# Kernel optimization log

Measured on AMD Instinct MI355X. Metric: run time of the kernel, lower is better.

The kernel has to match this reference:

```python
import jax, jax.numpy as jnp
import numpy as np

N = 50000
E = 600000
D = 128
BN_EPS = 1e-5
GIN_EPS = 0.0  # init_eps=0, not learned


def setup_inputs() -> dict:
    key = jax.random.key(0)
    ks = jax.random.split(key, 8)
    x = jax.random.normal(ks[0], (N, D), dtype=jnp.float32)
    edge_index = jax.random.randint(ks[1], (2, E), 0, N, dtype=jnp.int64)
    s = 1.0 / np.sqrt(D)
    w1 = jax.random.uniform(ks[2], (D, D), jnp.float32, -s, s)
    b1 = jax.random.uniform(ks[3], (D,), jnp.float32, -s, s)
    w2 = jax.random.uniform(ks[4], (D, D), jnp.float32, -s, s)
    b2 = jax.random.uniform(ks[5], (D,), jnp.float32, -s, s)
    gamma = jnp.ones((D,), jnp.float32)
    beta = jnp.zeros((D,), jnp.float32)
    return {"x": x, "edge_index": edge_index, "w1": w1, "b1": b1,
            "w2": w2, "b2": b2, "gamma": gamma, "beta": beta}


def reference(x, edge_index, w1, b1, w2, b2, gamma, beta):
    src, dst = edge_index[0], edge_index[1]
    # GINConv sum aggregation: out[i] = sum_{(j,i) in E} x[j]
    agg = jax.ops.segment_sum(x[src], dst, num_segments=N)  # [N, D]
    h = (1.0 + GIN_EPS) * x + agg
    # 2-layer MLP (Linear-ReLU-Linear)
    h = jax.nn.relu(h @ w1 + b1)
    h = h @ w2 + b2
    # training-mode BatchNorm over nodes (biased variance)
    mean = jnp.mean(h, axis=0)
    var = jnp.var(h, axis=0)
    h = (h - mean) * jax.lax.rsqrt(var + BN_EPS) * gamma + beta
    h = jax.nn.relu(h)
    # residual (in_dim == out_dim); dropout p=0.0 -> identity
    return x + h
```

## Files before the change

### kernel.cpp

```cpp
#include <hip/hip_runtime.h>

#define NN 50000
#define EE 600000
#define DD 128
#define MTILE 64
#define LDSTR 136
#define MAXDEG 64
#define NSLICE 32

typedef __attribute__((ext_vector_type(8))) short short8;
typedef __attribute__((ext_vector_type(4))) float f32x4;

static __device__ __forceinline__ unsigned short f2bf(float f) {
    unsigned int u = __float_as_uint(f);
    u += 0x7FFF + ((u >> 16) & 1);
    return (unsigned short)(u >> 16);
}
static __device__ __forceinline__ float bflo(unsigned int u) {
    return __uint_as_float(u << 16);
}
static __device__ __forceinline__ float bfhi(unsigned int u) {
    return __uint_as_float(u & 0xFFFF0000u);
}


__global__ __launch_bounds__(256) void k_prep(const float* __restrict__ w1,
                                              const float* __restrict__ w2,
                                              const float* __restrict__ x,
                                              unsigned short* __restrict__ wt,
                                              unsigned int* __restrict__ xb) {
    int tid = blockIdx.x * 256 + threadIdx.x;
    if (tid < 32768) {
        int w = tid >> 14, idx = tid & 16383;
        int k = idx >> 7, n = idx & 127;
        const float* src = w ? w2 : w1;
        wt[w * 16384 + n * 128 + k] = f2bf(src[k * 128 + n]);
    }
    int xi = tid - 32768;
    if (xi >= 0 && xi < NN * DD / 2) {
        float2 v = ((const float2*)x)[xi];
        xb[xi] = (unsigned int)f2bf(v.x) | ((unsigned int)f2bf(v.y) << 16);
    }
}


__global__ void k_scatter(const int* __restrict__ ei, int* __restrict__ cursor,
                          int* __restrict__ srcPad) {
    int e = blockIdx.x * blockDim.x + threadIdx.x;
    if (e < EE) {
        int s = ei[e];
        int d = ei[EE + e];
        int pos = atomicAdd(&cursor[d], 1);
        if (pos < MAXDEG) srcPad[(d << 6) + pos] = s;
    }
}


__global__ __launch_bounds__(256) void k_agg(const unsigned int* __restrict__ xb,
                                             const int* __restrict__ cursor,
                                             const int* srcPad,
                                             unsigned int* h0) {
    int wave = (blockIdx.x * blockDim.x + threadIdx.x) >> 6;
    int lane = threadIdx.x & 63;
    if (wave >= NN) return;
    int cnt = cursor[wave];
    if (cnt > MAXDEG) cnt = MAXDEG;
    int sv = srcPad[(wave << 6) + lane];
    unsigned int self = xb[(wave << 6) + lane];
    float ax = bflo(self), ay = bfhi(self);
    int j = 0;
    for (; j + 4 <= cnt; j += 4) {
        int a0 = __shfl(sv, j, 64);
        int a1 = __shfl(sv, j + 1, 64);
        int a2 = __shfl(sv, j + 2, 64);
        int a3 = __shfl(sv, j + 3, 64);
        unsigned int u0 = xb[(a0 << 6) + lane];
        unsigned int u1 = xb[(a1 << 6) + lane];
        unsigned int u2 = xb[(a2 << 6) + lane];
        unsigned int u3 = xb[(a3 << 6) + lane];
        ax += bflo(u0) + bflo(u1) + bflo(u2) + bflo(u3);
        ay += bfhi(u0) + bfhi(u1) + bfhi(u2) + bfhi(u3);
    }
    for (; j < cnt; ++j) {
        int s = __shfl(sv, j, 64);
        unsigned int u = xb[(s << 6) + lane];
        ax += bflo(u);
        ay += bfhi(u);
    }
    h0[(wave << 6) + lane] = (unsigned int)f2bf(ax) | ((unsigned int)f2bf(ay) << 16);
}


__global__ __launch_bounds__(256) void k_gemm(const unsigned short* __restrict__ A,
                                              const unsigned short* __restrict__ W,
                                              const float* __restrict__ bias,
                                              unsigned short* __restrict__ Cb,
                                              float* __restrict__ Cf,
                                              float* __restrict__ priv,
                                              int relu_bf16) {
    __shared__ __align__(16) unsigned short As[MTILE * LDSTR];
    __shared__ __align__(16) unsigned short Ws[128 * LDSTR];
    int t = threadIdx.x;
    int row0 = blockIdx.x * MTILE;

    #pragma unroll
    for (int i = 0; i < 8; ++i) {
        int idx = i * 256 + t;
        int r = idx >> 4, c = idx & 15;
        *(short8*)&Ws[r * LDSTR + c * 8] = *(const short8*)&W[r * 128 + c * 8];
    }
    #pragma unroll
    for (int i = 0; i < 4; ++i) {
        int idx = i * 256 + t;
        int r = idx >> 4, c = idx & 15;
        int gr = row0 + r;
        short8 v = (short8)0;
        if (gr < NN) v = *(const short8*)&A[gr * 128 + c * 8];
        *(short8*)&As[r * LDSTR + c * 8] = v;
    }
    __syncthreads();

    int lane = t & 63, wid = t >> 6;
    int m = lane & 15, quad = lane >> 4;
    f32x4 acc[8];
    #pragma unroll
    for (int i = 0; i < 8; ++i) acc[i] = (f32x4)0.f;

    #pragma unroll
    for (int kc = 0; kc < 4; ++kc) {
        int ko = kc * 32 + quad * 8;
        short8 af = *(const short8*)&As[(wid * 16 + m) * LDSTR + ko];
        #pragma unroll
        for (int nt = 0; nt < 8; ++nt) {
            short8 bfr = *(const short8*)&Ws[(nt * 16 + m) * LDSTR + ko];
            acc[nt] = __builtin_amdgcn_mfma_f32_16x16x32_bf16(af, bfr, acc[nt], 0, 0, 0);
        }
    }

    if (relu_bf16) {
        #pragma unroll
        for (int nt = 0; nt < 8; ++nt) {
            int col = nt * 16 + m;
            float bv = bias[col];
            #pragma unroll
            for (int r = 0; r < 4; ++r) {
                int gr = row0 + wid * 16 + quad * 4 + r;
                if (gr < NN) Cb[gr * 128 + col] = f2bf(fmaxf(acc[nt][r] + bv, 0.f));
            }
        }
    } else {
        float* myslice = priv + ((blockIdx.x * 4 + wid) & (NSLICE - 1)) * 2 * DD;
        #pragma unroll
        for (int nt = 0; nt < 8; ++nt) {
            int col = nt * 16 + m;
            float bv = bias[col];
            float s = 0.f, sq = 0.f;
            #pragma unroll
            for (int r = 0; r < 4; ++r) {
                int gr = row0 + wid * 16 + quad * 4 + r;
                if (gr < NN) {
                    float v = acc[nt][r] + bv;
                    Cf[gr * 128 + col] = v;
                    s += v;
                    sq += v * v;
                }
            }
            s  += __shfl_down(s, 32, 64);  sq += __shfl_down(sq, 32, 64);
            s  += __shfl_down(s, 16, 64);  sq += __shfl_down(sq, 16, 64);
            if (quad == 0) {
                atomicAdd(&myslice[col], s);
                atomicAdd(&myslice[DD + col], sq);
            }
        }
    }
}


__global__ __launch_bounds__(256) void k_bnred(const float* __restrict__ priv,
                                               float* __restrict__ stats) {
    int t = threadIdx.x;
    float acc = 0.f;
    #pragma unroll
    for (int s = 0; s < NSLICE; ++s) acc += priv[s * 2 * DD + t];
    stats[t] = acc;
}


__global__ __launch_bounds__(256) void k_final(const float* __restrict__ x,
                                               float* __restrict__ h,
                                               const float* __restrict__ stats,
                                               const float* __restrict__ gamma,
                                               const float* __restrict__ beta) {
    __shared__ float ssc[DD], ssh[DD];
    int t = threadIdx.x;
    if (t < DD) {
        float mean = stats[t] * (1.0f / NN);
        float var = fmaxf(stats[DD + t] * (1.0f / NN) - mean * mean, 0.f);
        float sc = gamma[t] * rsqrtf(var + 1e-5f);
        ssc[t] = sc;
        ssh[t] = beta[t] - mean * sc;
    }
    __syncthreads();
    int idx = blockIdx.x * 256 + t;
    if (idx >= NN * DD / 4) return;
    int c0 = (idx & 31) * 4;
    float4 hv = ((const float4*)h)[idx];
    float4 xv = ((const float4*)x)[idx];
    float4 o;
    o.x = xv.x + fmaxf(fmaf(hv.x, ssc[c0 + 0], ssh[c0 + 0]), 0.f);
    o.y = xv.y + fmaxf(fmaf(hv.y, ssc[c0 + 1], ssh[c0 + 1]), 0.f);
    o.z = xv.z + fmaxf(fmaf(hv.z, ssc[c0 + 2], ssh[c0 + 2]), 0.f);
    o.w = xv.w + fmaxf(fmaf(hv.w, ssc[c0 + 3], ssh[c0 + 3]), 0.f);
    ((float4*)h)[idx] = o;
}

extern "C" void kernel_launch(void* const* d_in, const int* in_sizes, int n_in,
                              void* d_out, int out_size, void* d_ws, size_t ws_size,
                              hipStream_t stream) {
    (void)in_sizes; (void)n_in; (void)out_size; (void)ws_size;
    const float* x     = (const float*)d_in[0];
    const int*   ei    = (const int*)d_in[1];
    const float* w1    = (const float*)d_in[2];
    const float* b1    = (const float*)d_in[3];
    const float* w2    = (const float*)d_in[4];
    const float* b2    = (const float*)d_in[5];
    const float* gamma = (const float*)d_in[6];
    const float* beta  = (const float*)d_in[7];
    float* out = (float*)d_out;

    char* wsb = (char*)d_ws;
    int*   cursor  = (int*)(wsb);
    int*   srcPad  = (int*)(wsb + 0x40000);
    unsigned int*   h0w = (unsigned int*)srcPad;
    unsigned short* h0b = (unsigned short*)srcPad;
    unsigned int*   xb  = (unsigned int*)(wsb + 0xD00000);
    unsigned short* h1b = (unsigned short*)xb;
    unsigned short* wt  = (unsigned short*)(wsb + 0x1940000);
    float* stats   = (float*)(wsb + 0x1960000);
    float* priv    = (float*)(wsb + 0x1961000);

    (void)hipMemsetAsync(cursor, 0, NN * sizeof(int), stream);
    (void)hipMemsetAsync(priv, 0, NSLICE * 2 * DD * sizeof(float), stream);

    k_prep<<<(32768 + NN * DD / 2 + 255) / 256, 256, 0, stream>>>(w1, w2, x, wt, xb);
    k_scatter<<<(EE + 255) / 256, 256, 0, stream>>>(ei, cursor, srcPad);
    k_agg<<<(NN * 64 + 255) / 256, 256, 0, stream>>>(xb, cursor, srcPad, h0w);
    k_gemm<<<(NN + MTILE - 1) / MTILE, 256, 0, stream>>>(h0b, wt, b1, h1b, nullptr, nullptr, 1);
    k_gemm<<<(NN + MTILE - 1) / MTILE, 256, 0, stream>>>(h1b, wt + 16384, b2, nullptr, out, priv, 0);
    k_bnred<<<1, 256, 0, stream>>>(priv, stats);
    k_final<<<(NN * DD / 4 + 255) / 256, 256, 0, stream>>>(x, out, stats, gamma, beta);
}
```

Before: 211.9 us.

## Fuse scatter into prep, enlarge GEMM tile, store bf16 pre-BN, fold BN reduce

Merges the edge-scatter kernel into the prep kernel and folds the BN slice reduction into the final kernel, removing two launches. The GEMM tile grows to 128 rows so each wave computes two 16-row MFMA tiles that share the same weight fragments. The second GEMM now writes its pre-BN output as bf16 to workspace instead of fp32 to the output buffer, which cuts intermediate traffic at some precision cost. The aggregation loop is unrolled by 8 for more loads in flight, and the final kernel processes four float4 elements per thread.

```diff
diff --git a/kernel.cpp b/kernel.cpp
--- a/kernel.cpp
+++ b/kernel.cpp
@@ -3,7 +3,7 @@
 #define NN 50000
 #define EE 600000
 #define DD 128
-#define MTILE 64
+#define MTILE 128
 #define LDSTR 136
 #define MAXDEG 64
 #define NSLICE 32
@@ -27,9 +27,18 @@
 __global__ __launch_bounds__(256) void k_prep(const float* __restrict__ w1,
                                               const float* __restrict__ w2,
                                               const float* __restrict__ x,
+                                              const int* __restrict__ ei,
+                                              int* __restrict__ cursor,
+                                              int* __restrict__ srcPad,
                                               unsigned short* __restrict__ wt,
                                               unsigned int* __restrict__ xb) {
     int tid = blockIdx.x * 256 + threadIdx.x;
+    if (tid < EE) {
+        int s = ei[tid];
+        int d = ei[EE + tid];
+        int pos = atomicAdd(&cursor[d], 1);
+        if (pos < MAXDEG) srcPad[(d << 6) + pos] = s;
+    }
     if (tid < 32768) {
         int w = tid >> 14, idx = tid & 16383;
         int k = idx >> 7, n = idx & 127;
@@ -40,18 +49,6 @@
     if (xi >= 0 && xi < NN * DD / 2) {
         float2 v = ((const float2*)x)[xi];
         xb[xi] = (unsigned int)f2bf(v.x) | ((unsigned int)f2bf(v.y) << 16);
-    }
-}
-
-
-__global__ void k_scatter(const int* __restrict__ ei, int* __restrict__ cursor,
-                          int* __restrict__ srcPad) {
-    int e = blockIdx.x * blockDim.x + threadIdx.x;
-    if (e < EE) {
-        int s = ei[e];
-        int d = ei[EE + e];
-        int pos = atomicAdd(&cursor[d], 1);
-        if (pos < MAXDEG) srcPad[(d << 6) + pos] = s;
     }
 }
 
@@ -69,15 +66,25 @@
     unsigned int self = xb[(wave << 6) + lane];
     float ax = bflo(self), ay = bfhi(self);
     int j = 0;
+    for (; j + 8 <= cnt; j += 8) {
+        int a0 = __shfl(sv, j, 64),     a1 = __shfl(sv, j + 1, 64);
+        int a2 = __shfl(sv, j + 2, 64), a3 = __shfl(sv, j + 3, 64);
+        int a4 = __shfl(sv, j + 4, 64), a5 = __shfl(sv, j + 5, 64);
+        int a6 = __shfl(sv, j + 6, 64), a7 = __shfl(sv, j + 7, 64);
+        unsigned int u0 = xb[(a0 << 6) + lane], u1 = xb[(a1 << 6) + lane];
+        unsigned int u2 = xb[(a2 << 6) + lane], u3 = xb[(a3 << 6) + lane];
+        unsigned int u4 = xb[(a4 << 6) + lane], u5 = xb[(a5 << 6) + lane];
+        unsigned int u6 = xb[(a6 << 6) + lane], u7 = xb[(a7 << 6) + lane];
+        ax += bflo(u0) + bflo(u1) + bflo(u2) + bflo(u3)
+            + bflo(u4) + bflo(u5) + bflo(u6) + bflo(u7);
+        ay += bfhi(u0) + bfhi(u1) + bfhi(u2) + bfhi(u3)
+            + bfhi(u4) + bfhi(u5) + bfhi(u6) + bfhi(u7);
+    }
     for (; j + 4 <= cnt; j += 4) {
-        int a0 = __shfl(sv, j, 64);
-        int a1 = __shfl(sv, j + 1, 64);
-        int a2 = __shfl(sv, j + 2, 64);
-        int a3 = __shfl(sv, j + 3, 64);
-        unsigned int u0 = xb[(a0 << 6) + lane];
-        unsigned int u1 = xb[(a1 << 6) + lane];
-        unsigned int u2 = xb[(a2 << 6) + lane];
-        unsigned int u3 = xb[(a3 << 6) + lane];
+        int a0 = __shfl(sv, j, 64),     a1 = __shfl(sv, j + 1, 64);
+        int a2 = __shfl(sv, j + 2, 64), a3 = __shfl(sv, j + 3, 64);
+        unsigned int u0 = xb[(a0 << 6) + lane], u1 = xb[(a1 << 6) + lane];
+        unsigned int u2 = xb[(a2 << 6) + lane], u3 = xb[(a3 << 6) + lane];
         ax += bflo(u0) + bflo(u1) + bflo(u2) + bflo(u3);
         ay += bfhi(u0) + bfhi(u1) + bfhi(u2) + bfhi(u3);
     }
@@ -95,9 +102,8 @@
                                               const unsigned short* __restrict__ W,
                                               const float* __restrict__ bias,
                                               unsigned short* __restrict__ Cb,
-                                              float* __restrict__ Cf,
                                               float* __restrict__ priv,
-                                              int relu_bf16) {
+                                              int relu) {
     __shared__ __align__(16) unsigned short As[MTILE * LDSTR];
     __shared__ __align__(16) unsigned short Ws[128 * LDSTR];
     int t = threadIdx.x;
@@ -110,7 +116,7 @@
         *(short8*)&Ws[r * LDSTR + c * 8] = *(const short8*)&W[r * 128 + c * 8];
     }
     #pragma unroll
-    for (int i = 0; i < 4; ++i) {
+    for (int i = 0; i < 8; ++i) {
         int idx = i * 256 + t;
         int r = idx >> 4, c = idx & 15;
         int gr = row0 + r;
@@ -122,31 +128,37 @@
 
     int lane = t & 63, wid = t >> 6;
     int m = lane & 15, quad = lane >> 4;
-    f32x4 acc[8];
-    #pragma unroll
-    for (int i = 0; i < 8; ++i) acc[i] = (f32x4)0.f;
+    f32x4 acc[2][8];
+    #pragma unroll
+    for (int mt = 0; mt < 2; ++mt)
+        #pragma unroll
+        for (int i = 0; i < 8; ++i) acc[mt][i] = (f32x4)0.f;
 
     #pragma unroll
     for (int kc = 0; kc < 4; ++kc) {
         int ko = kc * 32 + quad * 8;
-        short8 af = *(const short8*)&As[(wid * 16 + m) * LDSTR + ko];
+        short8 af0 = *(const short8*)&As[(wid * 32 + m) * LDSTR + ko];
+        short8 af1 = *(const short8*)&As[(wid * 32 + 16 + m) * LDSTR + ko];
         #pragma unroll
         for (int nt = 0; nt < 8; ++nt) {
             short8 bfr = *(const short8*)&Ws[(nt * 16 + m) * LDSTR + ko];
-            acc[nt] = __builtin_amdgcn_mfma_f32_16x16x32_bf16(af, bfr, acc[nt], 0, 0, 0);
-        }
-    }
-
-    if (relu_bf16) {
+            acc[0][nt] = __builtin_amdgcn_mfma_f32_16x16x32_bf16(af0, bfr, acc[0][nt], 0, 0, 0);
+            acc[1][nt] = __builtin_amdgcn_mfma_f32_16x16x32_bf16(af1, bfr, acc[1][nt], 0, 0, 0);
+        }
+    }
+
+    if (relu) {
         #pragma unroll
         for (int nt = 0; nt < 8; ++nt) {
             int col = nt * 16 + m;
             float bv = bias[col];
             #pragma unroll
-            for (int r = 0; r < 4; ++r) {
-                int gr = row0 + wid * 16 + quad * 4 + r;
-                if (gr < NN) Cb[gr * 128 + col] = f2bf(fmaxf(acc[nt][r] + bv, 0.f));
-            }
+            for (int mt = 0; mt < 2; ++mt)
+                #pragma unroll
+                for (int r = 0; r < 4; ++r) {
+                    int gr = row0 + wid * 32 + mt * 16 + quad * 4 + r;
+                    if (gr < NN) Cb[gr * 128 + col] = f2bf(fmaxf(acc[mt][nt][r] + bv, 0.f));
+                }
         }
     } else {
         float* myslice = priv + ((blockIdx.x * 4 + wid) & (NSLICE - 1)) * 2 * DD;
@@ -156,15 +168,17 @@
             float bv = bias[col];
             float s = 0.f, sq = 0.f;
             #pragma unroll
-            for (int r = 0; r < 4; ++r) {
-                int gr = row0 + wid * 16 + quad * 4 + r;
-                if (gr < NN) {
-                    float v = acc[nt][r] + bv;
-                    Cf[gr * 128 + col] = v;
-                    s += v;
-                    sq += v * v;
+            for (int mt = 0; mt < 2; ++mt)
+                #pragma unroll
+                for (int r = 0; r < 4; ++r) {
+                    int gr = row0 + wid * 32 + mt * 16 + quad * 4 + r;
+                    if (gr < NN) {
+                        float v = acc[mt][nt][r] + bv;
+                        Cb[gr * 128 + col] = f2bf(v);
+                        s += v;
+                        sq += v * v;
+                    }
                 }
-            }
             s  += __shfl_down(s, 32, 64);  sq += __shfl_down(sq, 32, 64);
             s  += __shfl_down(s, 16, 64);  sq += __shfl_down(sq, 16, 64);
             if (quad == 0) {
@@ -176,42 +190,43 @@
 }
 
 
-__global__ __launch_bounds__(256) void k_bnred(const float* __restrict__ priv,
-                                               float* __restrict__ stats) {
-    int t = threadIdx.x;
-    float acc = 0.f;
-    #pragma unroll
-    for (int s = 0; s < NSLICE; ++s) acc += priv[s * 2 * DD + t];
-    stats[t] = acc;
-}
-
-
 __global__ __launch_bounds__(256) void k_final(const float* __restrict__ x,
-                                               float* __restrict__ h,
-                                               const float* __restrict__ stats,
+                                               const unsigned int* __restrict__ h2,
+                                               float* __restrict__ out,
+                                               const float* __restrict__ priv,
                                                const float* __restrict__ gamma,
                                                const float* __restrict__ beta) {
     __shared__ float ssc[DD], ssh[DD];
     int t = threadIdx.x;
     if (t < DD) {
-        float mean = stats[t] * (1.0f / NN);
-        float var = fmaxf(stats[DD + t] * (1.0f / NN) - mean * mean, 0.f);
+        float s = 0.f, sq = 0.f;
+        #pragma unroll
+        for (int sl = 0; sl < NSLICE; ++sl) {
+            s  += priv[sl * 2 * DD + t];
+            sq += priv[sl * 2 * DD + DD + t];
+        }
+        float mean = s * (1.0f / NN);
+        float var = fmaxf(sq * (1.0f / NN) - mean * mean, 0.f);
         float sc = gamma[t] * rsqrtf(var + 1e-5f);
         ssc[t] = sc;
         ssh[t] = beta[t] - mean * sc;
     }
     __syncthreads();
-    int idx = blockIdx.x * 256 + t;
-    if (idx >= NN * DD / 4) return;
-    int c0 = (idx & 31) * 4;
-    float4 hv = ((const float4*)h)[idx];
-    float4 xv = ((const float4*)x)[idx];
-    float4 o;
-    o.x = xv.x + fmaxf(fmaf(hv.x, ssc[c0 + 0], ssh[c0 + 0]), 0.f);
-    o.y = xv.y + fmaxf(fmaf(hv.y, ssc[c0 + 1], ssh[c0 + 1]), 0.f);
-    o.z = xv.z + fmaxf(fmaf(hv.z, ssc[c0 + 2], ssh[c0 + 2]), 0.f);
-    o.w = xv.w + fmaxf(fmaf(hv.w, ssc[c0 + 3], ssh[c0 + 3]), 0.f);
-    ((float4*)h)[idx] = o;
+    #pragma unroll
+    for (int u = 0; u < 4; ++u) {
+        int idx = blockIdx.x * 1024 + u * 256 + t;
+        if (idx >= NN * DD / 4) return;
+        int c0 = (idx & 31) * 4;
+        unsigned int p0 = h2[2 * idx];
+        unsigned int p1 = h2[2 * idx + 1];
+        float4 xv = ((const float4*)x)[idx];
+        float4 o;
+        o.x = xv.x + fmaxf(fmaf(bflo(p0), ssc[c0 + 0], ssh[c0 + 0]), 0.f);
+        o.y = xv.y + fmaxf(fmaf(bfhi(p0), ssc[c0 + 1], ssh[c0 + 1]), 0.f);
+        o.z = xv.z + fmaxf(fmaf(bflo(p1), ssc[c0 + 2], ssh[c0 + 2]), 0.f);
+        o.w = xv.w + fmaxf(fmaf(bfhi(p1), ssc[c0 + 3], ssh[c0 + 3]), 0.f);
+        ((float4*)out)[idx] = o;
+    }
 }
 
 extern "C" void kernel_launch(void* const* d_in, const int* in_sizes, int n_in,
@@ -233,20 +248,19 @@
     int*   srcPad  = (int*)(wsb + 0x40000);
     unsigned int*   h0w = (unsigned int*)srcPad;
     unsigned short* h0b = (unsigned short*)srcPad;
+    unsigned short* h2b = (unsigned short*)srcPad;
+    unsigned int*   h2w = (unsigned int*)srcPad;
     unsigned int*   xb  = (unsigned int*)(wsb + 0xD00000);
     unsigned short* h1b = (unsigned short*)xb;
     unsigned short* wt  = (unsigned short*)(wsb + 0x1940000);
-    float* stats   = (float*)(wsb + 0x1960000);
-    float* priv    = (float*)(wsb + 0x1961000);
+    float* priv    = (float*)(wsb + 0x1960000);
 
     (void)hipMemsetAsync(cursor, 0, NN * sizeof(int), stream);
     (void)hipMemsetAsync(priv, 0, NSLICE * 2 * DD * sizeof(float), stream);
 
-    k_prep<<<(32768 + NN * DD / 2 + 255) / 256, 256, 0, stream>>>(w1, w2, x, wt, xb);
-    k_scatter<<<(EE + 255) / 256, 256, 0, stream>>>(ei, cursor, srcPad);
+    k_prep<<<(32768 + NN * DD / 2 + 255) / 256, 256, 0, stream>>>(w1, w2, x, ei, cursor, srcPad, wt, xb);
     k_agg<<<(NN * 64 + 255) / 256, 256, 0, stream>>>(xb, cursor, srcPad, h0w);
-    k_gemm<<<(NN + MTILE - 1) / MTILE, 256, 0, stream>>>(h0b, wt, b1, h1b, nullptr, nullptr, 1);
-    k_gemm<<<(NN + MTILE - 1) / MTILE, 256, 0, stream>>>(h1b, wt + 16384, b2, nullptr, out, priv, 0);
-    k_bnred<<<1, 256, 0, stream>>>(priv, stats);
-    k_final<<<(NN * DD / 4 + 255) / 256, 256, 0, stream>>>(x, out, stats, gamma, beta);
-}
+    k_gemm<<<(NN + MTILE - 1) / MTILE, 256, 0, stream>>>(h0b, wt, b1, h1b, nullptr, 1);
+    k_gemm<<<(NN + MTILE - 1) / MTILE, 256, 0, stream>>>(h1b, wt + 16384, b2, h2b, priv, 0);
+    k_final<<<(NN * DD / 4 + 1023) / 1024, 256, 0, stream>>>(x, h2w, out, priv, gamma, beta);
+}
```

After: 202.2 us. 1.05x faster.
